# Performance work log

Measured on AMD Instinct MI355X. Metric: run time of the kernel, lower is better.

Reference implementation:

```python
import jax, jax.numpy as jnp
import numpy as np

B, S, H, C, T = 8, 1024, 256, 4, 12
THETA = 10000.0


def setup_inputs() -> dict:
    key = jax.random.key(0)
    ks = jax.random.split(key, 7)
    x = jax.random.normal(ks[0], (B, S, H), dtype=jnp.float32)
    token_index = jax.random.randint(ks[1], (B, S), 0, 256, dtype=jnp.int32)
    thread_id = jnp.sort(jax.random.randint(ks[2], (B, S), 0, T, dtype=jnp.int32), axis=-1)
    bound = 1.0 / np.sqrt(H)  # nn.Linear default init range
    Wq = jax.random.uniform(ks[3], (H, H * C), jnp.float32, -bound, bound)
    bq = jax.random.uniform(ks[4], (H * C,), jnp.float32, -bound, bound)
    Wk = jax.random.uniform(ks[5], (H, H * C), jnp.float32, -bound, bound)
    bk = jax.random.uniform(ks[6], (H * C,), jnp.float32, -bound, bound)
    return {"x": x, "Wq": Wq, "bq": bq, "Wk": Wk, "bk": bk,
            "token_index": token_index, "thread_id": thread_id}


def _rope(v, pos):
    # v: (B, S, C, H); pos: (B, S) signed positions
    half = v.shape[-1] // 2
    # freqs = 1 / theta^(arange(0, H, 2) / H)
    freqs = 1.0 / (THETA ** (jnp.arange(half, dtype=jnp.float32) * 2.0 / (2 * half)))
    ang = pos[..., None].astype(jnp.float32) * freqs          # (B, S, half)
    cos = jnp.cos(ang)[:, :, None, :]                          # (B, S, 1, half)
    sin = jnp.sin(ang)[:, :, None, :]
    vr = v.reshape(*v.shape[:-1], half, 2)                     # complex pairs (even, odd)
    re = vr[..., 0] * cos - vr[..., 1] * sin
    im = vr[..., 0] * sin + vr[..., 1] * cos
    return jnp.stack([re, im], axis=-1).reshape(v.shape)


def reference(x, Wq, bq, Wk, bk, token_index, thread_id):
    q = (x @ Wq + bq).reshape(B, S, C, H)
    k = (x @ Wk + bk).reshape(B, S, C, H)
    # Block sign rules of get_instance_embedding reduce to three cases per
    # token pair (m, n) with thread ids ti=thread(m), tj=thread(n):
    #   0 < ti < tj : q uses -pos, k uses +pos
    #   0 < tj < ti : q uses +pos, k uses -pos
    #   otherwise   : both use +pos
    q_pos = _rope(q, token_index)
    q_neg = _rope(q, -token_index)
    k_pos = _rope(k, token_index)
    k_neg = _rope(k, -token_index)
    l1 = jnp.einsum('bmch,bnch->bcmn', q_pos, k_pos)
    l2 = jnp.einsum('bmch,bnch->bcmn', q_neg, k_pos)
    l3 = jnp.einsum('bmch,bnch->bcmn', q_pos, k_neg)
    ti = thread_id[:, :, None]   # rows
    tj = thread_id[:, None, :]   # cols
    cond2 = ((ti > 0) & (ti < tj))[:, None, :, :]   # (B,1,S,S)
    cond3 = ((tj > 0) & (ti > tj))[:, None, :, :]
    return jnp.where(cond2, l2, jnp.where(cond3, l3, l1))  # (B, C, S, S)
```

## Files before the change

### kernel.cpp

```cpp
#include <hip/hip_runtime.h>

#define BB 8
#define SS 1024
#define HH 256
#define CC 4
#define NQ 1024

typedef unsigned short u16;
typedef unsigned int u32;
typedef __attribute__((ext_vector_type(8))) __bf16 bf16x8;
typedef __attribute__((ext_vector_type(4))) float f32x4;
typedef __attribute__((ext_vector_type(4))) u32 u32x4;
typedef __attribute__((ext_vector_type(4))) u16 u16x4;

__device__ __forceinline__ u16 f2bf(float f) {
    u32 u = __float_as_uint(f);
    u32 r = (u + 0x7FFFu + ((u >> 16) & 1u)) >> 16;
    return (u16)r;
}

__device__ __forceinline__ void gld16(const u16* g, u16* l) {
    __builtin_amdgcn_global_load_lds(
        (const __attribute__((address_space(1))) void*)g,
        (__attribute__((address_space(3))) void*)l, 16, 0, 0);
}

__device__ __forceinline__ bf16x8 ldsfrag(const u16* smem, int row, int c16) {
    const char* p = (const char*)smem + row * 128 + (((c16 ^ (row & 7)) & 7) << 4);
    return *(const bf16x8*)p;
}

__global__ void k0_castx(const float4* __restrict__ x, u16x4* __restrict__ xbf) {
    int i = blockIdx.x * 256 + threadIdx.x;
    float4 v = x[i];
    u16x4 o = {f2bf(v.x), f2bf(v.y), f2bf(v.z), f2bf(v.w)};
    xbf[i] = o;
}

__global__ void k0_transw(const float* __restrict__ Wq, const float* __restrict__ Wk,
                          u16* __restrict__ Wt) {
    __shared__ u16 tl[64][65];
    int nb = blockIdx.x * 64, kb = blockIdx.y * 64;
    int c = threadIdx.x & 63;
#pragma unroll
    for (int r = threadIdx.x >> 6; r < 64; r += 4) {
        int k = kb + r, n = nb + c;
        float v = (n < NQ) ? Wq[k * NQ + n] : Wk[k * NQ + (n - NQ)];
        tl[c][r] = f2bf(v);
    }
    __syncthreads();
#pragma unroll
    for (int r = threadIdx.x >> 6; r < 64; r += 4) {
        Wt[(size_t)(nb + r) * HH + kb + c] = tl[r][c];
    }
}

__global__ void k0_trig(float2* __restrict__ trig) {
    int i = blockIdx.x * 256 + threadIdx.x;
    int pos = i >> 7, f = i & 127;
    float freq = __expf(-(float)f * 0.07195578515529633f);
    float ang = (float)pos * freq;
    float s, c;
    sincosf(ang, &s, &c);
    trig[i] = make_float2(c, s);
}

#define STAGE2(dst, srcbase, roff, kc)                                          \
    _Pragma("unroll") for (int i_ = 0; i_ < 2; ++i_) {                          \
        int r_ = ww * 16 + i_ * 8 + (l >> 3);                                   \
        int c16_ = (l & 7) ^ (r_ & 7);                                          \
        gld16((srcbase) + (size_t)((roff) + r_) * HH + (kc) * 64 + c16_ * 8,    \
              (dst) + (ww * 16 + i_ * 8) * 64);                                 \
    }

__global__ void __launch_bounds__(512, 2) k1_proj(
    const u16* __restrict__ xbf, const u16* __restrict__ Wt,
    const float* __restrict__ bq, const float* __restrict__ bk,
    const int* __restrict__ tok, const float2* __restrict__ trig,
    u16* __restrict__ qpos, u16* __restrict__ qneg,
    u16* __restrict__ kpos, u16* __restrict__ kneg) {
    int h = blockIdx.x;
    int logical = (h & 7) * 128 + (h >> 3);
    int m0 = (logical >> 4) * 128, n0 = (logical & 15) * 128;
    int ww = threadIdx.x >> 6, l = threadIdx.x & 63;
    int wr = ww >> 1, wc = ww & 1;

    __shared__ u16 sm[32768];
    u16* Ab[2] = {sm, sm + 16384};
    u16* Bb[2] = {sm + 8192, sm + 24576};

    f32x4 acc[2][4] = {};
    STAGE2(Ab[0], xbf, m0, 0)
    STAGE2(Bb[0], Wt, n0, 0)
    asm volatile("s_waitcnt vmcnt(0)" ::: "memory");
    __builtin_amdgcn_s_barrier();
#pragma unroll
    for (int kc = 0; kc < 4; ++kc) {
        u16* As = Ab[kc & 1];
        u16* Bs = Bb[kc & 1];
        if (kc < 3) {
            STAGE2(Ab[(kc + 1) & 1], xbf, m0, kc + 1)
            STAGE2(Bb[(kc + 1) & 1], Wt, n0, kc + 1)
        }
#pragma unroll
        for (int ks = 0; ks < 2; ++ks) {
            int c16 = (l >> 4) + ks * 4;
            bf16x8 af[2], bfr[4];
#pragma unroll
            for (int mi = 0; mi < 2; ++mi) af[mi] = ldsfrag(As, wr * 32 + mi * 16 + (l & 15), c16);
#pragma unroll
            for (int ns = 0; ns < 4; ++ns) bfr[ns] = ldsfrag(Bs, wc * 64 + ns * 16 + (l & 15), c16);
#pragma unroll
            for (int mi = 0; mi < 2; ++mi)
#pragma unroll
                for (int ns = 0; ns < 4; ++ns)
                    acc[mi][ns] = __builtin_amdgcn_mfma_f32_16x16x32_bf16(af[mi], bfr[ns], acc[mi][ns], 0, 0, 0);
        }
        if (kc < 3) {
            asm volatile("s_waitcnt vmcnt(0) lgkmcnt(0)" ::: "memory");
            __builtin_amdgcn_s_barrier();
        }
    }

#pragma unroll
    for (int mi = 0; mi < 2; ++mi)
#pragma unroll
        for (int ns = 0; ns < 4; ++ns) {
            int n = n0 + wc * 64 + ns * 16 + (l & 15);
            bool isq = n < NQ;
            int nc = n & (NQ - 1);
            float bias = isq ? bq[nc] : bk[nc];
            int c = nc >> 8, hh = nc & 255, fi = hh >> 1;
#pragma unroll
            for (int r = 0; r < 4; ++r) {
                int m = m0 + wr * 32 + mi * 16 + (l >> 4) * 4 + r;
                float val = acc[mi][ns][r] + bias;
                float other = __shfl_xor(val, 1);
                int pos = tok[m];
                float2 cs = trig[pos * 128 + fi];
                float rp, rn;
                if ((l & 1) == 0) {
                    rp = val * cs.x - other * cs.y;
                    rn = val * cs.x + other * cs.y;
                } else {
                    rp = other * cs.y + val * cs.x;
                    rn = -other * cs.y + val * cs.x;
                }
                int b = m >> 10, s = m & 1023;
                size_t oidx = ((size_t)((b << 2) | c) * SS + s) * HH + hh;
                if (isq) {
                    qpos[oidx] = f2bf(rp);
                    qneg[oidx] = f2bf(rn);
                } else {
                    kpos[oidx] = f2bf(rp);
                    kneg[oidx] = f2bf(rn);
                }
            }
        }
}

__global__ void __launch_bounds__(512, 2) k2_gemm(
    const u16* __restrict__ qpos, const u16* __restrict__ qneg,
    const u16* __restrict__ kpos, const u16* __restrict__ kneg,
    const int* __restrict__ thread_id, float* __restrict__ out) {
    int h = blockIdx.x;
    int logical = (h & 7) * 256 + (h >> 3);
    int bc = logical >> 6;
    int t = logical & 63;
    int m0 = (t >> 3) * 128, n0 = (t & 7) * 128;
    const int* tb = thread_id + (bc >> 2) * SS;
    int ww = threadIdx.x >> 6, l = threadIdx.x & 63;
    int wr = ww >> 1, wc = ww & 1;
    int ti0 = tb[m0], ti1 = tb[m0 + 127], tj0 = tb[n0], tj1 = tb[n0 + 127];
    bool pure2 = (ti0 > 0) & (ti1 < tj0);
    bool pure3 = (tj0 > 0) & (ti0 > tj1);
    bool pure1 = (ti1 == 0) | (tj1 == 0) | ((ti0 == ti1) & (tj0 == tj1) & (ti0 == tj0));
    size_t base = (size_t)bc * (SS * HH);
    float* ob = out + (size_t)bc * ((size_t)SS * SS);
    int ar0 = m0 + wr * 32;
    int nb0 = n0 + wc * 64;

    __shared__ u16 sm[32768];

    if (pure1 | pure2 | pure3) {
        const u16* q = (pure2 ? qneg : qpos) + base;
        const u16* k = (pure3 ? kneg : kpos) + base;
        u16* Ab[2] = {sm, sm + 16384};
        u16* Bb[2] = {sm + 8192, sm + 24576};

        f32x4 acc[2][4] = {};
        STAGE2(Ab[0], q, m0, 0)
        STAGE2(Bb[0], k, n0, 0)
        asm volatile("s_waitcnt vmcnt(0)" ::: "memory");
        __builtin_amdgcn_s_barrier();
#pragma unroll
        for (int kc = 0; kc < 4; ++kc) {
            u16* As = Ab[kc & 1];
            u16* Bs = Bb[kc & 1];
            if (kc < 3) {
                STAGE2(Ab[(kc + 1) & 1], q, m0, kc + 1)
                STAGE2(Bb[(kc + 1) & 1], k, n0, kc + 1)
            }
#pragma unroll
            for (int ks = 0; ks < 2; ++ks) {
                int c16 = (l >> 4) + ks * 4;
                bf16x8 af[2], bfr[4];
#pragma unroll
                for (int mi = 0; mi < 2; ++mi) af[mi] = ldsfrag(As, wr * 32 + mi * 16 + (l & 15), c16);
#pragma unroll
                for (int ns = 0; ns < 4; ++ns) bfr[ns] = ldsfrag(Bs, wc * 64 + ns * 16 + (l & 15), c16);
#pragma unroll
                for (int mi = 0; mi < 2; ++mi)
#pragma unroll
                    for (int ns = 0; ns < 4; ++ns)
                        acc[mi][ns] = __builtin_amdgcn_mfma_f32_16x16x32_bf16(af[mi], bfr[ns], acc[mi][ns], 0, 0, 0);
            }
            if (kc < 3) {
                asm volatile("s_waitcnt vmcnt(0) lgkmcnt(0)" ::: "memory");
                __builtin_amdgcn_s_barrier();
            }
        }

#pragma unroll
        for (int mi = 0; mi < 2; ++mi)
#pragma unroll
            for (int ns = 0; ns < 4; ++ns)
#pragma unroll
                for (int r = 0; r < 4; ++r) {
                    int m = ar0 + mi * 16 + (l >> 4) * 4 + r;
                    int n = nb0 + ns * 16 + (l & 15);
                    ob[(size_t)m * SS + n] = acc[mi][ns][r];
                }
    } else {
        const u16* qp = qpos + base;
        const u16* qn = qneg + base;
        const u16* kp = kpos + base;
        const u16* kn = kneg + base;
        u16* smqp = sm;
        u16* smqn = sm + 8192;
        u16* smkp = sm + 16384;
        u16* smkn = sm + 24576;

        int bamin = ti0 > 1 ? ti0 : 1;
        int bcmin = tj0 > 1 ? tj0 : 1;
        bool B2 = (ti1 > 0) && (tj1 > bamin);
        bool B3 = (tj1 > 0) && (ti1 > bcmin);

        int fa[2], fb[2], fc[4], fd[4];
#pragma unroll
        for (int mi = 0; mi < 2; ++mi) {
            fa[mi] = tb[ar0 + mi * 16];
            fb[mi] = tb[ar0 + mi * 16 + 15];
        }
#pragma unroll
        for (int ns = 0; ns < 4; ++ns) {
            fc[ns] = tb[nb0 + ns * 16];
            fd[ns] = tb[nb0 + ns * 16 + 15];
        }
        u32 msk1 = 0, msk2 = 0, msk3 = 0;
#pragma unroll
        for (int mi = 0; mi < 2; ++mi)
#pragma unroll
            for (int ns = 0; ns < 4; ++ns) {
                u32 bit = 1u << (mi * 4 + ns);
                if ((fa[mi] == 0) | (fc[ns] == 0) | ((fa[mi] <= fd[ns]) & (fc[ns] <= fb[mi]))) msk1 |= bit;
                int amin = fa[mi] > 1 ? fa[mi] : 1;
                if ((fb[mi] > 0) & (fd[ns] > amin)) msk2 |= bit;
                int cmin = fc[ns] > 1 ? fc[ns] : 1;
                if ((fd[ns] > 0) & (fb[mi] > cmin)) msk3 |= bit;
            }
        msk1 = __builtin_amdgcn_readfirstlane(msk1);
        msk2 = __builtin_amdgcn_readfirstlane(msk2);
        msk3 = __builtin_amdgcn_readfirstlane(msk3);

        f32x4 a1[2][4] = {}, a2[2][4] = {}, a3[2][4] = {};
        for (int kc = 0; kc < 4; ++kc) {
            if (kc) __builtin_amdgcn_s_barrier();
            STAGE2(smqp, qp, m0, kc)
            if (B2) STAGE2(smqn, qn, m0, kc)
            STAGE2(smkp, kp, n0, kc)
            if (B3) STAGE2(smkn, kn, n0, kc)
            asm volatile("s_waitcnt vmcnt(0)" ::: "memory");
            __builtin_amdgcn_s_barrier();
#pragma unroll
            for (int ks = 0; ks < 2; ++ks) {
                int c16 = (l >> 4) + ks * 4;
                bf16x8 qpF[2], qnF[2], kpF[4], knF[4];
#pragma unroll
                for (int mi = 0; mi < 2; ++mi) {
                    int rr = wr * 32 + mi * 16 + (l & 15);
                    qpF[mi] = ldsfrag(smqp, rr, c16);
                    if (msk2) qnF[mi] = ldsfrag(smqn, rr, c16);
                }
#pragma unroll
                for (int ns = 0; ns < 4; ++ns) {
                    int rn = wc * 64 + ns * 16 + (l & 15);
                    kpF[ns] = ldsfrag(smkp, rn, c16);
                    if (msk3) knF[ns] = ldsfrag(smkn, rn, c16);
                }
#pragma unroll
                for (int mi = 0; mi < 2; ++mi)
#pragma unroll
                    for (int ns = 0; ns < 4; ++ns) {
                        u32 bit = 1u << (mi * 4 + ns);
                        if (msk1 & bit)
                            a1[mi][ns] = __builtin_amdgcn_mfma_f32_16x16x32_bf16(qpF[mi], kpF[ns], a1[mi][ns], 0, 0, 0);
                        if (msk2 & bit)
                            a2[mi][ns] = __builtin_amdgcn_mfma_f32_16x16x32_bf16(qnF[mi], kpF[ns], a2[mi][ns], 0, 0, 0);
                        if (msk3 & bit)
                            a3[mi][ns] = __builtin_amdgcn_mfma_f32_16x16x32_bf16(qpF[mi], knF[ns], a3[mi][ns], 0, 0, 0);
                    }
            }
        }

        int tj[4], ti_[2][4];
#pragma unroll
        for (int ns = 0; ns < 4; ++ns) tj[ns] = tb[nb0 + ns * 16 + (l & 15)];
#pragma unroll
        for (int mi = 0; mi < 2; ++mi)
#pragma unroll
            for (int r = 0; r < 4; ++r) ti_[mi][r] = tb[ar0 + mi * 16 + (l >> 4) * 4 + r];

#pragma unroll
        for (int mi = 0; mi < 2; ++mi)
#pragma unroll
            for (int ns = 0; ns < 4; ++ns)
#pragma unroll
                for (int r = 0; r < 4; ++r) {
                    int m = ar0 + mi * 16 + (l >> 4) * 4 + r;
                    int n = nb0 + ns * 16 + (l & 15);
                    int ti = ti_[mi][r], tjj = tj[ns];
                    float v = (ti > 0 && ti < tjj) ? a2[mi][ns][r]
                             : ((tjj > 0 && ti > tjj) ? a3[mi][ns][r] : a1[mi][ns][r]);
                    ob[(size_t)m * SS + n] = v;
                }
    }
}

extern "C" void kernel_launch(void* const* d_in, const int* in_sizes, int n_in,
                              void* d_out, int out_size, void* d_ws, size_t ws_size,
                              hipStream_t stream) {
    const float* x  = (const float*)d_in[0];
    const float* Wq = (const float*)d_in[1];
    const float* bq = (const float*)d_in[2];
    const float* Wk = (const float*)d_in[3];
    const float* bk = (const float*)d_in[4];
    const int* tok  = (const int*)d_in[5];
    const int* tid  = (const int*)d_in[6];
    float* out = (float*)d_out;

    char* ws = (char*)d_ws;
    const size_t MB = 1u << 20;
    u16* qpos = (u16*)(ws);
    u16* qneg = (u16*)(ws + 16 * MB);
    u16* kpos = (u16*)(ws + 32 * MB);
    u16* kneg = (u16*)(ws + 48 * MB);
    u16* xbf  = (u16*)(ws + 64 * MB);
    u16* Wt   = (u16*)(ws + 68 * MB);
    float2* trig = (float2*)(ws + 69 * MB);

    k0_castx<<<2048, 256, 0, stream>>>((const float4*)x, (u16x4*)xbf);
    dim3 tg(32, 4);
    k0_transw<<<tg, 256, 0, stream>>>(Wq, Wk, Wt);
    k0_trig<<<128, 256, 0, stream>>>(trig);
    k1_proj<<<1024, 512, 0, stream>>>(xbf, Wt, bq, bk, tok, trig, qpos, qneg, kpos, kneg);
    k2_gemm<<<2048, 512, 0, stream>>>(qpos, qneg, kpos, kneg, tid, out);
}
```

Measured before the change: 123.5 us.

## Deepen prefetch to two stages and double-buffer the mixed-sign tile path

Reworks the K-loop staging in the projection GEMM and the pure-case logits GEMM so that two K chunks are in flight. The next load is issued only after the barrier that frees the buffer, and waits use partial vmcnt counts instead of draining all loads. The mixed-sign path, which was single-buffered with a full stall per chunk, now uses 32-wide K chunks double-buffered across 8 steps with a new swizzled 64-byte-row layout. MFMA sections are wrapped in s_setprio. The cost is an extra barrier per iteration and hand-counted vmcnt values that depend on which optional loads are issued.

Result: faster. 115.3 us (-6.7%).

```diff
diff --git a/kernel.cpp b/kernel.cpp
--- a/kernel.cpp
+++ b/kernel.cpp
@@ -29,6 +29,13 @@
     const char* p = (const char*)smem + row * 128 + (((c16 ^ (row & 7)) & 7) << 4);
     return *(const bf16x8*)p;
 }
+__device__ __forceinline__ bf16x8 ldsfrag32(const u16* smem, int row, int c16) {
+    const char* p = (const char*)smem + row * 64 + (((c16 ^ ((row >> 1) & 3)) & 3) << 4);
+    return *(const bf16x8*)p;
+}
+
+#define WAITV(n) asm volatile("s_waitcnt vmcnt(" #n ")" ::: "memory")
+#define WAITLG() asm volatile("s_waitcnt lgkmcnt(0)" ::: "memory")
 
 __global__ void k0_castx(const float4* __restrict__ x, u16x4* __restrict__ xbf) {
     int i = blockIdx.x * 256 + threadIdx.x;
@@ -72,6 +79,13 @@
         gld16((srcbase) + (size_t)((roff) + r_) * HH + (kc) * 64 + c16_ * 8,    \
               (dst) + (ww * 16 + i_ * 8) * 64);                                 \
     }
+#define STAGE32(dst, srcbase, roff, kc) do {                                    \
+        int r_ = ww * 4 + (l >> 2) + 0 * 0;                                     \
+        r_ = (threadIdx.x >> 2);                                                \
+        int sl_ = (threadIdx.x & 3) ^ ((r_ >> 1) & 3);                          \
+        gld16((srcbase) + (size_t)((roff) + r_) * HH + (kc) * 32 + sl_ * 8,     \
+              (dst) + ww * 512);                                                \
+    } while (0)
 
 __global__ void __launch_bounds__(512, 2) k1_proj(
     const u16* __restrict__ xbf, const u16* __restrict__ Wt,
@@ -92,16 +106,15 @@
     f32x4 acc[2][4] = {};
     STAGE2(Ab[0], xbf, m0, 0)
     STAGE2(Bb[0], Wt, n0, 0)
-    asm volatile("s_waitcnt vmcnt(0)" ::: "memory");
+    STAGE2(Ab[1], xbf, m0, 1)
+    STAGE2(Bb[1], Wt, n0, 1)
+    WAITV(4);
     __builtin_amdgcn_s_barrier();
 #pragma unroll
     for (int kc = 0; kc < 4; ++kc) {
-        u16* As = Ab[kc & 1];
-        u16* Bs = Bb[kc & 1];
-        if (kc < 3) {
-            STAGE2(Ab[(kc + 1) & 1], xbf, m0, kc + 1)
-            STAGE2(Bb[(kc + 1) & 1], Wt, n0, kc + 1)
-        }
+        const u16* As = Ab[kc & 1];
+        const u16* Bs = Bb[kc & 1];
+        __builtin_amdgcn_s_setprio(1);
 #pragma unroll
         for (int ks = 0; ks < 2; ++ks) {
             int c16 = (l >> 4) + ks * 4;
@@ -116,8 +129,17 @@
                 for (int ns = 0; ns < 4; ++ns)
                     acc[mi][ns] = __builtin_amdgcn_mfma_f32_16x16x32_bf16(af[mi], bfr[ns], acc[mi][ns], 0, 0, 0);
         }
+        __builtin_amdgcn_s_setprio(0);
         if (kc < 3) {
-            asm volatile("s_waitcnt vmcnt(0) lgkmcnt(0)" ::: "memory");
+            WAITLG();
+            __builtin_amdgcn_s_barrier();
+            if (kc < 2) {
+                STAGE2(Ab[kc & 1], xbf, m0, kc + 2)
+                STAGE2(Bb[kc & 1], Wt, n0, kc + 2)
+                WAITV(4);
+            } else {
+                WAITV(0);
+            }
             __builtin_amdgcn_s_barrier();
         }
     }
@@ -191,16 +213,15 @@
         f32x4 acc[2][4] = {};
         STAGE2(Ab[0], q, m0, 0)
         STAGE2(Bb[0], k, n0, 0)
-        asm volatile("s_waitcnt vmcnt(0)" ::: "memory");
+        STAGE2(Ab[1], q, m0, 1)
+        STAGE2(Bb[1], k, n0, 1)
+        WAITV(4);
         __builtin_amdgcn_s_barrier();
 #pragma unroll
         for (int kc = 0; kc < 4; ++kc) {
-            u16* As = Ab[kc & 1];
-            u16* Bs = Bb[kc & 1];
-            if (kc < 3) {
-                STAGE2(Ab[(kc + 1) & 1], q, m0, kc + 1)
-                STAGE2(Bb[(kc + 1) & 1], k, n0, kc + 1)
-            }
+            const u16* As = Ab[kc & 1];
+            const u16* Bs = Bb[kc & 1];
+            __builtin_amdgcn_s_setprio(1);
 #pragma unroll
             for (int ks = 0; ks < 2; ++ks) {
                 int c16 = (l >> 4) + ks * 4;
@@ -215,8 +236,17 @@
                     for (int ns = 0; ns < 4; ++ns)
                         acc[mi][ns] = __builtin_amdgcn_mfma_f32_16x16x32_bf16(af[mi], bfr[ns], acc[mi][ns], 0, 0, 0);
             }
+            __builtin_amdgcn_s_setprio(0);
             if (kc < 3) {
-                asm volatile("s_waitcnt vmcnt(0) lgkmcnt(0)" ::: "memory");
+                WAITLG();
+                __builtin_amdgcn_s_barrier();
+                if (kc < 2) {
+                    STAGE2(Ab[kc & 1], q, m0, kc + 2)
+                    STAGE2(Bb[kc & 1], k, n0, kc + 2)
+                    WAITV(4);
+                } else {
+                    WAITV(0);
+                }
                 __builtin_amdgcn_s_barrier();
             }
         }
@@ -236,10 +266,7 @@
         const u16* qn = qneg + base;
         const u16* kp = kpos + base;
         const u16* kn = kneg + base;
-        u16* smqp = sm;
-        u16* smqn = sm + 8192;
-        u16* smkp = sm + 16384;
-        u16* smkn = sm + 24576;
+        u16* bufb[2] = {sm, sm + 16384};
 
         int bamin = ti0 > 1 ? ti0 : 1;
         int bcmin = tj0 > 1 ? tj0 : 1;
@@ -273,45 +300,71 @@
         msk2 = __builtin_amdgcn_readfirstlane(msk2);
         msk3 = __builtin_amdgcn_readfirstlane(msk3);
 
+#define MSTAGE(bi, kc) do {                                \
+        STAGE32(bufb[bi], qp, m0, kc);                     \
+        if (B2) STAGE32(bufb[bi] + 4096, qn, m0, kc);      \
+        STAGE32(bufb[bi] + 8192, kp, n0, kc);              \
+        if (B3) STAGE32(bufb[bi] + 12288, kn, n0, kc);     \
+    } while (0)
+#define WAITN() do {                                       \
+        if (B2 & B3) { WAITV(4); }                         \
+        else if (B2 | B3) { WAITV(3); }                    \
+        else { WAITV(2); }                                 \
+    } while (0)
+
         f32x4 a1[2][4] = {}, a2[2][4] = {}, a3[2][4] = {};
-        for (int kc = 0; kc < 4; ++kc) {
-            if (kc) __builtin_amdgcn_s_barrier();
-            STAGE2(smqp, qp, m0, kc)
-            if (B2) STAGE2(smqn, qn, m0, kc)
-            STAGE2(smkp, kp, n0, kc)
-            if (B3) STAGE2(smkn, kn, n0, kc)
-            asm volatile("s_waitcnt vmcnt(0)" ::: "memory");
-            __builtin_amdgcn_s_barrier();
-#pragma unroll
-            for (int ks = 0; ks < 2; ++ks) {
-                int c16 = (l >> 4) + ks * 4;
-                bf16x8 qpF[2], qnF[2], kpF[4], knF[4];
-#pragma unroll
-                for (int mi = 0; mi < 2; ++mi) {
-                    int rr = wr * 32 + mi * 16 + (l & 15);
-                    qpF[mi] = ldsfrag(smqp, rr, c16);
-                    if (msk2) qnF[mi] = ldsfrag(smqn, rr, c16);
-                }
+        MSTAGE(0, 0);
+        MSTAGE(1, 1);
+        WAITN();
+        __builtin_amdgcn_s_barrier();
+#pragma unroll
+        for (int kc = 0; kc < 8; ++kc) {
+            const u16* bqp = bufb[kc & 1];
+            const u16* bqn = bqp + 4096;
+            const u16* bkp = bqp + 8192;
+            const u16* bkn = bqp + 12288;
+            int c16 = l >> 4;
+            bf16x8 qpF[2], qnF[2], kpF[4], knF[4];
+            __builtin_amdgcn_s_setprio(1);
+#pragma unroll
+            for (int mi = 0; mi < 2; ++mi) {
+                int rr = wr * 32 + mi * 16 + (l & 15);
+                qpF[mi] = ldsfrag32(bqp, rr, c16);
+                if (msk2) qnF[mi] = ldsfrag32(bqn, rr, c16);
+            }
+#pragma unroll
+            for (int ns = 0; ns < 4; ++ns) {
+                int rn = wc * 64 + ns * 16 + (l & 15);
+                kpF[ns] = ldsfrag32(bkp, rn, c16);
+                if (msk3) knF[ns] = ldsfrag32(bkn, rn, c16);
+            }
+#pragma unroll
+            for (int mi = 0; mi < 2; ++mi)
 #pragma unroll
                 for (int ns = 0; ns < 4; ++ns) {
-                    int rn = wc * 64 + ns * 16 + (l & 15);
-                    kpF[ns] = ldsfrag(smkp, rn, c16);
-                    if (msk3) knF[ns] = ldsfrag(smkn, rn, c16);
-                }
-#pragma unroll
-                for (int mi = 0; mi < 2; ++mi)
-#pragma unroll
-                    for (int ns = 0; ns < 4; ++ns) {
-                        u32 bit = 1u << (mi * 4 + ns);
-                        if (msk1 & bit)
-                            a1[mi][ns] = __builtin_amdgcn_mfma_f32_16x16x32_bf16(qpF[mi], kpF[ns], a1[mi][ns], 0, 0, 0);
-                        if (msk2 & bit)
-                            a2[mi][ns] = __builtin_amdgcn_mfma_f32_16x16x32_bf16(qnF[mi], kpF[ns], a2[mi][ns], 0, 0, 0);
-                        if (msk3 & bit)
-                            a3[mi][ns] = __builtin_amdgcn_mfma_f32_16x16x32_bf16(qpF[mi], knF[ns], a3[mi][ns], 0, 0, 0);
-                    }
-            }
-        }
+                    u32 bit = 1u << (mi * 4 + ns);
+                    if (msk1 & bit)
+                        a1[mi][ns] = __builtin_amdgcn_mfma_f32_16x16x32_bf16(qpF[mi], kpF[ns], a1[mi][ns], 0, 0, 0);
+                    if (msk2 & bit)
+                        a2[mi][ns] = __builtin_amdgcn_mfma_f32_16x16x32_bf16(qnF[mi], kpF[ns], a2[mi][ns], 0, 0, 0);
+                    if (msk3 & bit)
+                        a3[mi][ns] = __builtin_amdgcn_mfma_f32_16x16x32_bf16(qpF[mi], knF[ns], a3[mi][ns], 0, 0, 0);
+                }
+            __builtin_amdgcn_s_setprio(0);
+            if (kc < 7) {
+                WAITLG();
+                __builtin_amdgcn_s_barrier();
+                if (kc < 6) {
+                    MSTAGE(kc & 1, kc + 2);
+                    WAITN();
+                } else {
+                    WAITV(0);
+                }
+                __builtin_amdgcn_s_barrier();
+            }
+        }
+#undef MSTAGE
+#undef WAITN
 
         int tj[4], ti_[2][4];
 #pragma unroll
```

## Retile score GEMM into 256x256 per-case passes with deeper prefetch

Applied to the files above, without the earlier changes.

The score kernel is restructured so that each block computes a 256x256 tile for a single sign case (pos/pos, neg/pos, pos/neg). A block exits early when its case cannot occur under the sorted thread ids, and otherwise writes only the elements its case owns. This replaces the old per-128-tile pure/mixed branching that kept three accumulators. Both GEMM kernels now prefetch two K-chunks ahead with partial vmcnt waits and raise wave priority around the MFMA loops. In exchange the score kernel needs 128KB of dynamic LDS and more accumulator registers per wave, and mixed tiles are read and computed up to three times with masked scattered stores.

Result: slower. 150.0 us (+21.5%).

```diff
diff --git a/kernel.cpp b/kernel.cpp
--- a/kernel.cpp
+++ b/kernel.cpp
@@ -29,6 +29,9 @@
     const char* p = (const char*)smem + row * 128 + (((c16 ^ (row & 7)) & 7) << 4);
     return *(const bf16x8*)p;
 }
+
+#define WAITV(n) asm volatile("s_waitcnt vmcnt(" #n ")" ::: "memory")
+#define WAITLG() asm volatile("s_waitcnt lgkmcnt(0)" ::: "memory")
 
 __global__ void k0_castx(const float4* __restrict__ x, u16x4* __restrict__ xbf) {
     int i = blockIdx.x * 256 + threadIdx.x;
@@ -71,6 +74,13 @@
         int c16_ = (l & 7) ^ (r_ & 7);                                          \
         gld16((srcbase) + (size_t)((roff) + r_) * HH + (kc) * 64 + c16_ * 8,    \
               (dst) + (ww * 16 + i_ * 8) * 64);                                 \
+    }
+#define STAGE4(dst, srcbase, roff, kc)                                          \
+    _Pragma("unroll") for (int i_ = 0; i_ < 4; ++i_) {                          \
+        int r_ = i_ * 64 + ww * 8 + (l >> 3);                                   \
+        int c16_ = (l & 7) ^ (r_ & 7);                                          \
+        gld16((srcbase) + (size_t)((roff) + r_) * HH + (kc) * 64 + c16_ * 8,    \
+              (dst) + (i_ * 64 + ww * 8) * 64);                                 \
     }
 
 __global__ void __launch_bounds__(512, 2) k1_proj(
@@ -92,16 +102,15 @@
     f32x4 acc[2][4] = {};
     STAGE2(Ab[0], xbf, m0, 0)
     STAGE2(Bb[0], Wt, n0, 0)
-    asm volatile("s_waitcnt vmcnt(0)" ::: "memory");
+    STAGE2(Ab[1], xbf, m0, 1)
+    STAGE2(Bb[1], Wt, n0, 1)
+    WAITV(4);
     __builtin_amdgcn_s_barrier();
 #pragma unroll
     for (int kc = 0; kc < 4; ++kc) {
-        u16* As = Ab[kc & 1];
-        u16* Bs = Bb[kc & 1];
-        if (kc < 3) {
-            STAGE2(Ab[(kc + 1) & 1], xbf, m0, kc + 1)
-            STAGE2(Bb[(kc + 1) & 1], Wt, n0, kc + 1)
-        }
+        const u16* As = Ab[kc & 1];
+        const u16* Bs = Bb[kc & 1];
+        __builtin_amdgcn_s_setprio(1);
 #pragma unroll
         for (int ks = 0; ks < 2; ++ks) {
             int c16 = (l >> 4) + ks * 4;
@@ -116,8 +125,17 @@
                 for (int ns = 0; ns < 4; ++ns)
                     acc[mi][ns] = __builtin_amdgcn_mfma_f32_16x16x32_bf16(af[mi], bfr[ns], acc[mi][ns], 0, 0, 0);
         }
+        __builtin_amdgcn_s_setprio(0);
         if (kc < 3) {
-            asm volatile("s_waitcnt vmcnt(0) lgkmcnt(0)" ::: "memory");
+            WAITLG();
+            __builtin_amdgcn_s_barrier();
+            if (kc < 2) {
+                STAGE2(Ab[kc & 1], xbf, m0, kc + 2)
+                STAGE2(Bb[kc & 1], Wt, n0, kc + 2)
+                WAITV(4);
+            } else {
+                WAITV(0);
+            }
             __builtin_amdgcn_s_barrier();
         }
     }
@@ -163,178 +181,98 @@
     const u16* __restrict__ qpos, const u16* __restrict__ qneg,
     const u16* __restrict__ kpos, const u16* __restrict__ kneg,
     const int* __restrict__ thread_id, float* __restrict__ out) {
-    int h = blockIdx.x;
-    int logical = (h & 7) * 256 + (h >> 3);
-    int bc = logical >> 6;
-    int t = logical & 63;
-    int m0 = (t >> 3) * 128, n0 = (t & 7) * 128;
+    int slot = blockIdx.x;
+    int logical = (slot & 7) * 192 + (slot >> 3);
+    int bc = logical / 48;
+    int rem = logical % 48;
+    int pass = rem >> 4;
+    int tile = rem & 15;
+    int m0 = (tile >> 2) * 256, n0 = (tile & 3) * 256;
     const int* tb = thread_id + (bc >> 2) * SS;
+
+    int ti0 = tb[m0], ti1 = tb[m0 + 255], tj0 = tb[n0], tj1 = tb[n0 + 255];
+    bool need;
+    if (pass == 0)      need = (ti0 == 0) | (tj0 == 0) | ((ti0 <= tj1) & (tj0 <= ti1));
+    else if (pass == 1) need = (ti1 > 0) && (tj1 > (ti0 > 0 ? ti0 : 1));
+    else                need = (tj1 > 0) && (ti1 > (tj0 > 0 ? tj0 : 1));
+    if (!need) return;
+
+    size_t base = (size_t)bc * (SS * HH);
+    const u16* q = (pass == 1 ? qneg : qpos) + base;
+    const u16* k = (pass == 2 ? kneg : kpos) + base;
+    float* ob = out + (size_t)bc * ((size_t)SS * SS);
+
     int ww = threadIdx.x >> 6, l = threadIdx.x & 63;
-    int wr = ww >> 1, wc = ww & 1;
-    int ti0 = tb[m0], ti1 = tb[m0 + 127], tj0 = tb[n0], tj1 = tb[n0 + 127];
-    bool pure2 = (ti0 > 0) & (ti1 < tj0);
-    bool pure3 = (tj0 > 0) & (ti0 > tj1);
-    bool pure1 = (ti1 == 0) | (tj1 == 0) | ((ti0 == ti1) & (tj0 == tj1) & (ti0 == tj0));
-    size_t base = (size_t)bc * (SS * HH);
-    float* ob = out + (size_t)bc * ((size_t)SS * SS);
-    int ar0 = m0 + wr * 32;
+    int wr = ww >> 2, wc = ww & 3;
+    int ar0 = m0 + wr * 128;
     int nb0 = n0 + wc * 64;
 
-    __shared__ u16 sm[32768];
-
-    if (pure1 | pure2 | pure3) {
-        const u16* q = (pure2 ? qneg : qpos) + base;
-        const u16* k = (pure3 ? kneg : kpos) + base;
-        u16* Ab[2] = {sm, sm + 16384};
-        u16* Bb[2] = {sm + 8192, sm + 24576};
-
-        f32x4 acc[2][4] = {};
-        STAGE2(Ab[0], q, m0, 0)
-        STAGE2(Bb[0], k, n0, 0)
-        asm volatile("s_waitcnt vmcnt(0)" ::: "memory");
-        __builtin_amdgcn_s_barrier();
-#pragma unroll
-        for (int kc = 0; kc < 4; ++kc) {
-            u16* As = Ab[kc & 1];
-            u16* Bs = Bb[kc & 1];
-            if (kc < 3) {
-                STAGE2(Ab[(kc + 1) & 1], q, m0, kc + 1)
-                STAGE2(Bb[(kc + 1) & 1], k, n0, kc + 1)
+    extern __shared__ u16 sm[];
+    u16* Ab[2] = {sm, sm + 32768};
+    u16* Bb[2] = {sm + 16384, sm + 49152};
+
+    f32x4 acc[8][4] = {};
+    STAGE4(Ab[0], q, m0, 0)
+    STAGE4(Bb[0], k, n0, 0)
+    STAGE4(Ab[1], q, m0, 1)
+    STAGE4(Bb[1], k, n0, 1)
+    WAITV(8);
+    __builtin_amdgcn_s_barrier();
+#pragma unroll
+    for (int kc = 0; kc < 4; ++kc) {
+        const u16* As = Ab[kc & 1];
+        const u16* Bs = Bb[kc & 1];
+        __builtin_amdgcn_s_setprio(1);
+#pragma unroll
+        for (int ks = 0; ks < 2; ++ks) {
+            int c16 = (l >> 4) + ks * 4;
+            bf16x8 af[8], bfr[4];
+#pragma unroll
+            for (int ns = 0; ns < 4; ++ns) bfr[ns] = ldsfrag(Bs, wc * 64 + ns * 16 + (l & 15), c16);
+#pragma unroll
+            for (int mi = 0; mi < 8; ++mi) af[mi] = ldsfrag(As, wr * 128 + mi * 16 + (l & 15), c16);
+#pragma unroll
+            for (int mi = 0; mi < 8; ++mi)
+#pragma unroll
+                for (int ns = 0; ns < 4; ++ns)
+                    acc[mi][ns] = __builtin_amdgcn_mfma_f32_16x16x32_bf16(af[mi], bfr[ns], acc[mi][ns], 0, 0, 0);
+        }
+        __builtin_amdgcn_s_setprio(0);
+        if (kc < 3) {
+            WAITLG();
+            __builtin_amdgcn_s_barrier();
+            if (kc < 2) {
+                STAGE4(Ab[kc & 1], q, m0, kc + 2)
+                STAGE4(Bb[kc & 1], k, n0, kc + 2)
+                WAITV(8);
+            } else {
+                WAITV(0);
             }
-#pragma unroll
-            for (int ks = 0; ks < 2; ++ks) {
-                int c16 = (l >> 4) + ks * 4;
-                bf16x8 af[2], bfr[4];
-#pragma unroll
-                for (int mi = 0; mi < 2; ++mi) af[mi] = ldsfrag(As, wr * 32 + mi * 16 + (l & 15), c16);
-#pragma unroll
-                for (int ns = 0; ns < 4; ++ns) bfr[ns] = ldsfrag(Bs, wc * 64 + ns * 16 + (l & 15), c16);
-#pragma unroll
-                for (int mi = 0; mi < 2; ++mi)
-#pragma unroll
-                    for (int ns = 0; ns < 4; ++ns)
-                        acc[mi][ns] = __builtin_amdgcn_mfma_f32_16x16x32_bf16(af[mi], bfr[ns], acc[mi][ns], 0, 0, 0);
-            }
-            if (kc < 3) {
-                asm volatile("s_waitcnt vmcnt(0) lgkmcnt(0)" ::: "memory");
-                __builtin_amdgcn_s_barrier();
-            }
-        }
-
-#pragma unroll
-        for (int mi = 0; mi < 2; ++mi)
-#pragma unroll
-            for (int ns = 0; ns < 4; ++ns)
-#pragma unroll
-                for (int r = 0; r < 4; ++r) {
-                    int m = ar0 + mi * 16 + (l >> 4) * 4 + r;
+            __builtin_amdgcn_s_barrier();
+        }
+    }
+
+    int tjv[4];
+#pragma unroll
+    for (int ns = 0; ns < 4; ++ns) tjv[ns] = tb[nb0 + ns * 16 + (l & 15)];
+#pragma unroll
+    for (int mi = 0; mi < 8; ++mi)
+#pragma unroll
+        for (int r = 0; r < 4; ++r) {
+            int m = ar0 + mi * 16 + (l >> 4) * 4 + r;
+            int ti = tb[m];
+#pragma unroll
+            for (int ns = 0; ns < 4; ++ns) {
+                int tj = tjv[ns];
+                bool c2 = (ti > 0) & (ti < tj);
+                bool c3 = (tj > 0) & (ti > tj);
+                bool wm = (pass == 0) ? !(c2 | c3) : ((pass == 1) ? c2 : c3);
+                if (wm) {
                     int n = nb0 + ns * 16 + (l & 15);
                     ob[(size_t)m * SS + n] = acc[mi][ns][r];
                 }
-    } else {
-        const u16* qp = qpos + base;
-        const u16* qn = qneg + base;
-        const u16* kp = kpos + base;
-        const u16* kn = kneg + base;
-        u16* smqp = sm;
-        u16* smqn = sm + 8192;
-        u16* smkp = sm + 16384;
-        u16* smkn = sm + 24576;
-
-        int bamin = ti0 > 1 ? ti0 : 1;
-        int bcmin = tj0 > 1 ? tj0 : 1;
-        bool B2 = (ti1 > 0) && (tj1 > bamin);
-        bool B3 = (tj1 > 0) && (ti1 > bcmin);
-
-        int fa[2], fb[2], fc[4], fd[4];
-#pragma unroll
-        for (int mi = 0; mi < 2; ++mi) {
-            fa[mi] = tb[ar0 + mi * 16];
-            fb[mi] = tb[ar0 + mi * 16 + 15];
-        }
-#pragma unroll
-        for (int ns = 0; ns < 4; ++ns) {
-            fc[ns] = tb[nb0 + ns * 16];
-            fd[ns] = tb[nb0 + ns * 16 + 15];
-        }
-        u32 msk1 = 0, msk2 = 0, msk3 = 0;
-#pragma unroll
-        for (int mi = 0; mi < 2; ++mi)
-#pragma unroll
-            for (int ns = 0; ns < 4; ++ns) {
-                u32 bit = 1u << (mi * 4 + ns);
-                if ((fa[mi] == 0) | (fc[ns] == 0) | ((fa[mi] <= fd[ns]) & (fc[ns] <= fb[mi]))) msk1 |= bit;
-                int amin = fa[mi] > 1 ? fa[mi] : 1;
-                if ((fb[mi] > 0) & (fd[ns] > amin)) msk2 |= bit;
-                int cmin = fc[ns] > 1 ? fc[ns] : 1;
-                if ((fd[ns] > 0) & (fb[mi] > cmin)) msk3 |= bit;
             }
-        msk1 = __builtin_amdgcn_readfirstlane(msk1);
-        msk2 = __builtin_amdgcn_readfirstlane(msk2);
-        msk3 = __builtin_amdgcn_readfirstlane(msk3);
-
-        f32x4 a1[2][4] = {}, a2[2][4] = {}, a3[2][4] = {};
-        for (int kc = 0; kc < 4; ++kc) {
-            if (kc) __builtin_amdgcn_s_barrier();
-            STAGE2(smqp, qp, m0, kc)
-            if (B2) STAGE2(smqn, qn, m0, kc)
-            STAGE2(smkp, kp, n0, kc)
-            if (B3) STAGE2(smkn, kn, n0, kc)
-            asm volatile("s_waitcnt vmcnt(0)" ::: "memory");
-            __builtin_amdgcn_s_barrier();
-#pragma unroll
-            for (int ks = 0; ks < 2; ++ks) {
-                int c16 = (l >> 4) + ks * 4;
-                bf16x8 qpF[2], qnF[2], kpF[4], knF[4];
-#pragma unroll
-                for (int mi = 0; mi < 2; ++mi) {
-                    int rr = wr * 32 + mi * 16 + (l & 15);
-                    qpF[mi] = ldsfrag(smqp, rr, c16);
-                    if (msk2) qnF[mi] = ldsfrag(smqn, rr, c16);
-                }
-#pragma unroll
-                for (int ns = 0; ns < 4; ++ns) {
-                    int rn = wc * 64 + ns * 16 + (l & 15);
-                    kpF[ns] = ldsfrag(smkp, rn, c16);
-                    if (msk3) knF[ns] = ldsfrag(smkn, rn, c16);
-                }
-#pragma unroll
-                for (int mi = 0; mi < 2; ++mi)
-#pragma unroll
-                    for (int ns = 0; ns < 4; ++ns) {
-                        u32 bit = 1u << (mi * 4 + ns);
-                        if (msk1 & bit)
-                            a1[mi][ns] = __builtin_amdgcn_mfma_f32_16x16x32_bf16(qpF[mi], kpF[ns], a1[mi][ns], 0, 0, 0);
-                        if (msk2 & bit)
-                            a2[mi][ns] = __builtin_amdgcn_mfma_f32_16x16x32_bf16(qnF[mi], kpF[ns], a2[mi][ns], 0, 0, 0);
-                        if (msk3 & bit)
-                            a3[mi][ns] = __builtin_amdgcn_mfma_f32_16x16x32_bf16(qpF[mi], knF[ns], a3[mi][ns], 0, 0, 0);
-                    }
-            }
-        }
-
-        int tj[4], ti_[2][4];
-#pragma unroll
-        for (int ns = 0; ns < 4; ++ns) tj[ns] = tb[nb0 + ns * 16 + (l & 15)];
-#pragma unroll
-        for (int mi = 0; mi < 2; ++mi)
-#pragma unroll
-            for (int r = 0; r < 4; ++r) ti_[mi][r] = tb[ar0 + mi * 16 + (l >> 4) * 4 + r];
-
-#pragma unroll
-        for (int mi = 0; mi < 2; ++mi)
-#pragma unroll
-            for (int ns = 0; ns < 4; ++ns)
-#pragma unroll
-                for (int r = 0; r < 4; ++r) {
-                    int m = ar0 + mi * 16 + (l >> 4) * 4 + r;
-                    int n = nb0 + ns * 16 + (l & 15);
-                    int ti = ti_[mi][r], tjj = tj[ns];
-                    float v = (ti > 0 && ti < tjj) ? a2[mi][ns][r]
-                             : ((tjj > 0 && ti > tjj) ? a3[mi][ns][r] : a1[mi][ns][r]);
-                    ob[(size_t)m * SS + n] = v;
-                }
-    }
+        }
 }
 
 extern "C" void kernel_launch(void* const* d_in, const int* in_sizes, int n_in,
@@ -364,5 +302,5 @@
     k0_transw<<<tg, 256, 0, stream>>>(Wq, Wk, Wt);
     k0_trig<<<128, 256, 0, stream>>>(trig);
     k1_proj<<<1024, 512, 0, stream>>>(xbf, Wt, bq, bk, tok, trig, qpos, qneg, kpos, kneg);
-    k2_gemm<<<2048, 512, 0, stream>>>(qpos, qneg, kpos, kneg, tid, out);
-}
+    k2_gemm<<<1536, 512, 131072, stream>>>(qpos, qneg, kpos, kneg, tid, out);
+}
```
